# Performance work log

Measured on AMD Instinct MI355X. Metric: run time of the kernel, lower is better.

The kernel has to match this reference:

```python
import jax, jax.numpy as jnp
import numpy as np

SCALE_H, SCALE_W = 160.0, 160.0  # init spatial_scale
ALIGNED = False


def setup_inputs() -> dict:
    key = jax.random.key(0)
    k1, k2, k3 = jax.random.split(key, 3)
    feats = jax.random.normal(k1, (4, 256, 160, 160), dtype=jnp.float32)
    B, N = 4, 512
    bidx = jax.random.randint(k2, (N,), 0, B).astype(jnp.float32)
    p = jax.random.uniform(k3, (N, 4), dtype=jnp.float32)
    x1 = p[:, 0] * 0.7
    y1 = p[:, 1] * 0.7
    x2 = x1 + 0.05 + p[:, 2] * 0.25
    y2 = y1 + 0.05 + p[:, 3] * 0.25
    rois = jnp.stack([bidx, x1, y1, x2, y2], axis=1)
    return {
        "input_images_or_features": feats,
        "rois": rois,
        "output_height": 14,
        "output_width": 14,
    }


def reference(input_images_or_features, rois, output_height, output_width):
    feats = input_images_or_features  # [B, C, H, W]
    B, C, H, W = feats.shape
    OH, OW = int(output_height), int(output_width)
    dt = rois.dtype

    b = rois[:, 0].astype(jnp.int32)                      # [N]
    x1 = rois[:, 1] * SCALE_W
    y1 = rois[:, 2] * SCALE_H
    x2 = rois[:, 3] * SCALE_W
    y2 = rois[:, 4] * SCALE_H
    rw = x2 - x1
    rh = y2 - y1

    xs = jnp.arange(OW, dtype=dt) / max(OW - 1, 1)
    ys = jnp.arange(OH, dtype=dt) / max(OH - 1, 1)
    gy, gx = jnp.meshgrid(ys, xs, indexing="ij")          # [OH, OW]

    fx = x1[:, None, None] + gx[None] * rw[:, None, None]  # [N, OH, OW]
    fy = y1[:, None, None] + gy[None] * rh[:, None, None]

    if ALIGNED:
        nfx = fx / (W - 1) * 2 - 1
        nfy = fy / (H - 1) * 2 - 1
        ix = (nfx + 1) / 2 * (W - 1)
        iy = (nfy + 1) / 2 * (H - 1)
    else:
        nfx = fx / W * 2 - 1
        nfy = fy / H * 2 - 1
        ix = ((nfx + 1) * W - 1) / 2
        iy = ((nfy + 1) * H - 1) / 2

    x0f = jnp.floor(ix)
    y0f = jnp.floor(iy)
    x0 = x0f.astype(jnp.int32)
    y0 = y0f.astype(jnp.int32)

    wx1 = ix - x0f   # weight for x0+1
    wx0 = 1.0 - wx1
    wy1 = iy - y0f
    wy0 = 1.0 - wy1

    bb = b[:, None, None]

    def corner(yi, xi, w):
        valid = (xi >= 0) & (xi < W) & (yi >= 0) & (yi < H)
        xc = jnp.clip(xi, 0, W - 1)
        yc = jnp.clip(yi, 0, H - 1)
        v = feats[bb, :, yc, xc]                 # [N, OH, OW, C]
        return v * (w * valid.astype(dt))[..., None]

    out = (corner(y0, x0, wy0 * wx0)
           + corner(y0, x0 + 1, wy0 * wx1)
           + corner(y0 + 1, x0, wy1 * wx0)
           + corner(y0 + 1, x0 + 1, wy1 * wx1))   # [N, OH, OW, C]
    return jnp.transpose(out, (0, 3, 1, 2))       # [N, C, OH, OW]
```

## Files before the change

kernel.cpp:

```cpp
#include <hip/hip_runtime.h>
#include <cstddef>
#include <cstring>

#define RA_C  256
#define RA_H  160
#define RA_W  160
#define RA_OH 14
#define RA_OW 14
#define RA_SCALE 160.0f
#define RA_K  8
#define RA_NXCD 8

__device__ __forceinline__ float2 ldg_f2(const float* p) {
    float2 r;
    __builtin_memcpy(&r, p, sizeof(float2));
    return r;
}

__global__ __launch_bounds__(256) void roi_align_kernel(
    const float* __restrict__ feats,
    const float* __restrict__ rois,
    float* __restrict__ out,
    int N,
    int bpc)
{
    constexpr int S   = RA_OH * RA_OW;
    constexpr int CG  = RA_C / RA_K;
    constexpr int CGX = CG / RA_NXCD;
    constexpr int HW  = RA_H * RA_W;

    int bid   = blockIdx.x;
    int xcd   = bid & (RA_NXCD - 1);
    int local = bid >> 3;
    int cg    = xcd * CGX + local / bpc;
    int rem   = local - (local / bpc) * bpc;

    int idx_in_cg = rem * 256 + (int)threadIdx.x;
    if (idx_in_cg >= N * S) return;

    int n = idx_in_cg / S;
    int s = idx_in_cg - n * S;
    int oy = s / RA_OW;
    int ox = s - oy * RA_OW;

    const float* r = rois + (size_t)n * 5;
    int   b  = (int)r[0];
    float x1 = r[1] * RA_SCALE;
    float y1 = r[2] * RA_SCALE;
    float rw = r[3] * RA_SCALE - x1;
    float rh = r[4] * RA_SCALE - y1;

    float gx = (float)ox * (1.0f / (RA_OW - 1));
    float gy = (float)oy * (1.0f / (RA_OH - 1));
    float fx = x1 + gx * rw;
    float fy = y1 + gy * rh;

    float nfx = fx / (float)RA_W * 2.0f - 1.0f;
    float nfy = fy / (float)RA_H * 2.0f - 1.0f;
    float ix  = ((nfx + 1.0f) * (float)RA_W - 1.0f) * 0.5f;
    float iy  = ((nfy + 1.0f) * (float)RA_H - 1.0f) * 0.5f;

    float x0f = floorf(ix), y0f = floorf(iy);
    int   x0  = (int)x0f,   y0  = (int)y0f;
    float wx1 = ix - x0f,   wx0 = 1.0f - wx1;
    float wy1 = iy - y0f,   wy0 = 1.0f - wy1;

    int xp = x0 + 1, yp = y0 + 1;
    bool vx0 = (x0 >= 0) && (x0 < RA_W);
    bool vx1 = (xp >= 0) && (xp < RA_W);
    bool vy0 = (y0 >= 0) && (y0 < RA_H);
    bool vy1 = (yp >= 0) && (yp < RA_H);

    float w00 = wy0 * wx0 * ((vy0 && vx0) ? 1.0f : 0.0f);
    float w01 = wy0 * wx1 * ((vy0 && vx1) ? 1.0f : 0.0f);
    float w10 = wy1 * wx0 * ((vy1 && vx0) ? 1.0f : 0.0f);
    float w11 = wy1 * wx1 * ((vy1 && vx1) ? 1.0f : 0.0f);

    int  px   = min(max(x0, 0), RA_W - 2);
    bool swp  = (x0 != px);
    float a0 = swp ? w01 : w00;
    float b0 = swp ? w00 : w01;
    float a1 = swp ? w11 : w10;
    float b1 = swp ? w10 : w11;

    int y0c = min(max(y0, 0), RA_H - 1);
    int y1c = min(max(yp, 0), RA_H - 1);
    int o0  = y0c * RA_W + px;
    int o1  = y1c * RA_W + px;

    int c0 = cg * RA_K;
    const float* fb = feats + ((size_t)b * RA_C + c0) * HW;
    float*       op = out   + ((size_t)n * RA_C + c0) * S + s;

#pragma unroll
    for (int k = 0; k < RA_K; ++k) {
        const float* f = fb + (size_t)k * HW;
        float2 p0 = ldg_f2(f + o0);
        float2 p1 = ldg_f2(f + o1);
        float v = fmaf(a0, p0.x, fmaf(b0, p0.y, fmaf(a1, p1.x, b1 * p1.y)));
        op[(size_t)k * S] = v;
    }
}

extern "C" void kernel_launch(void* const* d_in, const int* in_sizes, int n_in,
                              void* d_out, int out_size, void* d_ws, size_t ws_size,
                              hipStream_t stream) {
    const float* feats = (const float*)d_in[0];
    const float* rois  = (const float*)d_in[1];
    float*       out   = (float*)d_out;

    int N = in_sizes[1] / 5;
    constexpr int S  = RA_OH * RA_OW;
    constexpr int CG = RA_C / RA_K;

    int bpc  = (N * S + 255) / 256;
    int grid = CG * bpc;
    roi_align_kernel<<<grid, 256, 0, stream>>>(feats, rois, out, N, bpc);
}
```

Baseline: 232.2 us.

## Stage per-ROI feature window in LDS with coalesced float4 loads

Each block now handles one ROI and one group of four channels. It first copies the ROI's bounding feature window into shared memory with coalesced float4 loads, then the 196 output threads do bilinear interpolation from LDS. Outputs are written with nontemporal stores. This targets the scattered float2 gathers of the old per-output-thread design, at the cost of 48KB of LDS per block and a barrier. It also idles 60 of 256 threads during compute and reads whole window rows instead of only the sampled points.

```diff
diff --git a/kernel.cpp b/kernel.cpp
--- a/kernel.cpp
+++ b/kernel.cpp
@@ -1,19 +1,42 @@
 #include <hip/hip_runtime.h>
 #include <cstddef>
-#include <cstring>
 
-#define RA_C  256
-#define RA_H  160
-#define RA_W  160
-#define RA_OH 14
-#define RA_OW 14
+#define RA_C   256
+#define RA_H   160
+#define RA_W   160
+#define RA_OH  14
+#define RA_OW  14
+#define RA_S   196
 #define RA_SCALE 160.0f
-#define RA_K  8
+#define RA_K   4
+#define RA_CG  (RA_C / RA_K)
 #define RA_NXCD 8
+#define W_ROWS 50
+#define W_STR  60
 
-__device__ __forceinline__ float2 ldg_f2(const float* p) {
-    float2 r;
-    __builtin_memcpy(&r, p, sizeof(float2));
+struct XParam { int p; float w0, w1; };
+
+__device__ __forceinline__ XParam axis_param(float lo, float ext, int o,
+                                             float inv, int lim)
+{
+    float g   = (float)o * inv;
+    float f   = lo + g * ext;
+    float nf  = f / (float)lim * 2.0f - 1.0f;
+    float ix  = ((nf + 1.0f) * (float)lim - 1.0f) * 0.5f;
+    float i0f = floorf(ix);
+    int   i0  = (int)i0f;
+    float w1  = ix - i0f, w0 = 1.0f - w1;
+    bool  v0  = (i0 >= 0) && (i0 < lim);
+    int   ip  = i0 + 1;
+    bool  v1  = (ip >= 0) && (ip < lim);
+    float W0  = w0 * (v0 ? 1.0f : 0.0f);
+    float W1  = w1 * (v1 ? 1.0f : 0.0f);
+    int   p   = min(max(i0, 0), lim - 2);
+    bool  swp = (i0 != p);
+    XParam r;
+    r.p  = p;
+    r.w0 = swp ? W1 : W0;
+    r.w1 = swp ? W0 : W1;
     return r;
 }
 
@@ -21,27 +44,21 @@
     const float* __restrict__ feats,
     const float* __restrict__ rois,
     float* __restrict__ out,
-    int N,
-    int bpc)
+    int N)
 {
-    constexpr int S   = RA_OH * RA_OW;
-    constexpr int CG  = RA_C / RA_K;
-    constexpr int CGX = CG / RA_NXCD;
-    constexpr int HW  = RA_H * RA_W;
+    __shared__ __align__(16) float win[RA_K][W_ROWS][W_STR];
+
+    constexpr int HW = RA_H * RA_W;
+    constexpr float invx = 1.0f / (RA_OW - 1);
+    constexpr float invy = 1.0f / (RA_OH - 1);
 
     int bid   = blockIdx.x;
     int xcd   = bid & (RA_NXCD - 1);
     int local = bid >> 3;
-    int cg    = xcd * CGX + local / bpc;
-    int rem   = local - (local / bpc) * bpc;
-
-    int idx_in_cg = rem * 256 + (int)threadIdx.x;
-    if (idx_in_cg >= N * S) return;
-
-    int n = idx_in_cg / S;
-    int s = idx_in_cg - n * S;
-    int oy = s / RA_OW;
-    int ox = s - oy * RA_OW;
+    int cgl   = local / N;
+    int n     = local - cgl * N;
+    int cg    = xcd * (RA_CG / RA_NXCD) + cgl;
+    int tid   = (int)threadIdx.x;
 
     const float* r = rois + (size_t)n * 5;
     int   b  = (int)r[0];
@@ -50,55 +67,54 @@
     float rw = r[3] * RA_SCALE - x1;
     float rh = r[4] * RA_SCALE - y1;
 
-    float gx = (float)ox * (1.0f / (RA_OW - 1));
-    float gy = (float)oy * (1.0f / (RA_OH - 1));
-    float fx = x1 + gx * rw;
-    float fy = y1 + gy * rh;
+    int c0  = axis_param(x1, rw, 0,         invx, RA_W).p;
+    int c1  = axis_param(x1, rw, RA_OW - 1, invx, RA_W).p + 1;
+    int r0  = axis_param(y1, rh, 0,         invy, RA_H).p;
+    int r1  = axis_param(y1, rh, RA_OH - 1, invy, RA_H).p + 1;
+    int c0a   = c0 & ~3;
+    int nw4   = ((c1 - c0a) >> 2) + 1;
+    int nrows = r1 - r0 + 1;
 
-    float nfx = fx / (float)RA_W * 2.0f - 1.0f;
-    float nfy = fy / (float)RA_H * 2.0f - 1.0f;
-    float ix  = ((nfx + 1.0f) * (float)RA_W - 1.0f) * 0.5f;
-    float iy  = ((nfy + 1.0f) * (float)RA_H - 1.0f) * 0.5f;
-
-    float x0f = floorf(ix), y0f = floorf(iy);
-    int   x0  = (int)x0f,   y0  = (int)y0f;
-    float wx1 = ix - x0f,   wx0 = 1.0f - wx1;
-    float wy1 = iy - y0f,   wy0 = 1.0f - wy1;
-
-    int xp = x0 + 1, yp = y0 + 1;
-    bool vx0 = (x0 >= 0) && (x0 < RA_W);
-    bool vx1 = (xp >= 0) && (xp < RA_W);
-    bool vy0 = (y0 >= 0) && (y0 < RA_H);
-    bool vy1 = (yp >= 0) && (yp < RA_H);
-
-    float w00 = wy0 * wx0 * ((vy0 && vx0) ? 1.0f : 0.0f);
-    float w01 = wy0 * wx1 * ((vy0 && vx1) ? 1.0f : 0.0f);
-    float w10 = wy1 * wx0 * ((vy1 && vx0) ? 1.0f : 0.0f);
-    float w11 = wy1 * wx1 * ((vy1 && vx1) ? 1.0f : 0.0f);
-
-    int  px   = min(max(x0, 0), RA_W - 2);
-    bool swp  = (x0 != px);
-    float a0 = swp ? w01 : w00;
-    float b0 = swp ? w00 : w01;
-    float a1 = swp ? w11 : w10;
-    float b1 = swp ? w10 : w11;
-
-    int y0c = min(max(y0, 0), RA_H - 1);
-    int y1c = min(max(yp, 0), RA_H - 1);
-    int o0  = y0c * RA_W + px;
-    int o1  = y1c * RA_W + px;
-
-    int c0 = cg * RA_K;
-    const float* fb = feats + ((size_t)b * RA_C + c0) * HW;
-    float*       op = out   + ((size_t)n * RA_C + c0) * S + s;
-
+    const float* fbase = feats + ((size_t)b * RA_C + cg * RA_K) * HW;
+    int total4 = nrows * nw4;
+    unsigned mgc = (1u << 22) / (unsigned)nw4 + 1;
 #pragma unroll
     for (int k = 0; k < RA_K; ++k) {
-        const float* f = fb + (size_t)k * HW;
-        float2 p0 = ldg_f2(f + o0);
-        float2 p1 = ldg_f2(f + o1);
-        float v = fmaf(a0, p0.x, fmaf(b0, p0.y, fmaf(a1, p1.x, b1 * p1.y)));
-        op[(size_t)k * S] = v;
+        const float* fk = fbase + (size_t)k * HW;
+        for (int i = tid; i < total4; i += 256) {
+            int row = (int)(((unsigned)i * mgc) >> 22);
+            int j4  = (i - row * nw4) << 2;
+            float4 v = *(const float4*)(fk + (size_t)((r0 + row) * RA_W + c0a + j4));
+            *(float4*)&win[k][row][j4] = v;
+        }
+    }
+
+    float A0 = 0.f, B0 = 0.f, A1 = 0.f, B1 = 0.f;
+    int cx = 0, ry = 0;
+    if (tid < RA_S) {
+        int oy = tid / RA_OW;
+        int ox = tid - oy * RA_OW;
+        XParam xp = axis_param(x1, rw, ox, invx, RA_W);
+        XParam yp = axis_param(y1, rh, oy, invy, RA_H);
+        A0 = yp.w0 * xp.w0;  B0 = yp.w0 * xp.w1;
+        A1 = yp.w1 * xp.w0;  B1 = yp.w1 * xp.w1;
+        cx = xp.p - c0a;
+        ry = yp.p - r0;
+    }
+
+    __syncthreads();
+
+    if (tid < RA_S) {
+        float* obase = out + ((size_t)n * RA_C + cg * RA_K) * RA_S + tid;
+#pragma unroll
+        for (int k = 0; k < RA_K; ++k) {
+            const float* w0p = &win[k][ry][cx];
+            const float* w1p = &win[k][ry + 1][cx];
+            float p00 = w0p[0], p01 = w0p[1];
+            float p10 = w1p[0], p11 = w1p[1];
+            float v = fmaf(A0, p00, fmaf(B0, p01, fmaf(A1, p10, B1 * p11)));
+            __builtin_nontemporal_store(v, obase + (size_t)k * RA_S);
+        }
     }
 }
 
@@ -109,11 +125,7 @@
     const float* rois  = (const float*)d_in[1];
     float*       out   = (float*)d_out;
 
-    int N = in_sizes[1] / 5;
-    constexpr int S  = RA_OH * RA_OW;
-    constexpr int CG = RA_C / RA_K;
-
-    int bpc  = (N * S + 255) / 256;
-    int grid = CG * bpc;
-    roi_align_kernel<<<grid, 256, 0, stream>>>(feats, rois, out, N, bpc);
+    int N    = in_sizes[1] / 5;
+    int grid = N * RA_CG;
+    roi_align_kernel<<<grid, 256, 0, stream>>>(feats, rois, out, N);
 }
```

Result: slower. 290.7 us (+25.2%).
